# Kernel optimization log

Measured on AMD Instinct MI355X. Metric: run time of the kernel, lower is better.

## Reference

```python
import jax, jax.numpy as jnp
import numpy as np
from jax.scipy.special import logsumexp

SIGMA = 1.0
EPSILON = 1.0
MAX_ITER = 10


def _gaussian_kernel(x, y, sigma):
    # x: (b, l, d), y: (b, k, d) -> (b, l, k) negative-kernel matrix exp(-||x-y||^2 / (2 sigma^2))
    outer = jnp.einsum('bld,bkd->blk', x, y)
    norm_x = jnp.sum(x * x, axis=2)
    norm_y = jnp.sum(y * y, axis=2)
    dist = (norm_x[:, :, None] + norm_y[:, None, :] - 2.0 * outer) / (2.0 * sigma ** 2)
    return jnp.exp(-jnp.maximum(dist, 0.0))


def setup_inputs() -> dict:
    key = jax.random.key(0)
    kx, ka, ky, kb = jax.random.split(key, 4)
    B, L, K, D = 8, 2048, 2048, 32
    return {
        'x': jax.random.normal(kx, (B, L, D), dtype=jnp.float32),
        'a': jax.random.normal(ka, (B, L), dtype=jnp.float32),
        'y': jax.random.normal(ky, (B, K, D), dtype=jnp.float32),
        'b': jax.random.normal(kb, (B, K), dtype=jnp.float32),
    }


def _sinkhorn_potentials(x, a, y, b):
    sg = jax.lax.stop_gradient
    # Kernel matrices (carry gradient wrt x, y); weights a, b are detached inside kernels.
    Kxx = _gaussian_kernel(x, x, SIGMA) / EPSILON + sg(a)[:, None, :]
    Kyx_base = _gaussian_kernel(y, x, SIGMA)
    Kyx = Kyx_base / EPSILON + sg(a)[:, None, :]
    Kxy = jnp.swapaxes(Kyx_base, 1, 2) / EPSILON + sg(b)[:, None, :]
    Kyy = _gaussian_kernel(y, y, SIGMA) / EPSILON + sg(b)[:, None, :]

    # Sinkhorn loop runs under no_grad in the original: stop-gradient kernels.
    Kxx_s, Kyx_s, Kxy_s, Kyy_s = sg(Kxx), sg(Kyx), sg(Kxy), sg(Kyy)

    def step(carry, _):
        fxx, fyx, fxy, fyy = carry
        # sequential (Gauss-Seidel) update order matches the torch dict order xx, yx, xy, yy
        fxx = 0.5 * fxx - 0.5 * logsumexp(Kxx_s + fxx[:, None, :], axis=2)
        fyx = 0.5 * fyx - 0.5 * logsumexp(Kyx_s + fxy[:, None, :], axis=2)  # uses old fxy
        fxy = 0.5 * fxy - 0.5 * logsumexp(Kxy_s + fyx[:, None, :], axis=2)  # uses new fyx
        fyy = 0.5 * fyy - 0.5 * logsumexp(Kyy_s + fyy[:, None, :], axis=2)
        return (fxx, fyx, fxy, fyy), None

    init = (jnp.zeros_like(a), jnp.zeros_like(b), jnp.zeros_like(a), jnp.zeros_like(b))
    (fxx, fyx, fxy, fyy), _ = jax.lax.scan(step, init, None, length=MAX_ITER)

    # Final differentiable extrapolation step (potentials are detached constants).
    fe_xx = -logsumexp(Kxx + fxx[:, None, :], axis=2)
    fe_yx = -logsumexp(Kyx + fxy[:, None, :], axis=2)
    fe_xy = -logsumexp(Kxy + fyx[:, None, :], axis=2)
    fe_yy = -logsumexp(Kyy + fyy[:, None, :], axis=2)
    f = fe_xy - fe_xx  # (b, l)
    g = fe_yx - fe_yy  # (b, k)
    return f, g


def reference(x, a, y, b):
    f, g = _sinkhorn_potentials(x, a, y, b)
    res = jnp.sum(f * jnp.exp(a), axis=1) + jnp.sum(g * jnp.exp(b), axis=1)
    return res * EPSILON  # (batch,)
```

## Files before the change

kernel.cpp:

```cpp
#include <hip/hip_runtime.h>
#include <hip/hip_bf16.h>

#define B_ 8
#define N_ 2048
#define D_ 32
#define RCAP 16
#define EM1_DIAG 1.7182818284590452f
#define M_   8.0f
#define EM_  2980.9579870417283f
#define L2E  1.4426950408889634f
#define LN2  0.6931471805599453f
#define MH_  (0.5f * M_ * L2E)

typedef __attribute__((ext_vector_type(8))) short short8;
typedef __attribute__((ext_vector_type(4))) float f32x4;

__global__ void setup_kernel(const float* __restrict__ x, const float* __restrict__ y,
                             unsigned short* __restrict__ xb, unsigned short* __restrict__ yb,
                             float* __restrict__ NX, float* __restrict__ NY,
                             int* __restrict__ csr_cnt)
{
    int t = blockIdx.x * 256 + threadIdx.x;
    const float* src = (t < 16384) ? x : y;
    unsigned short* dstb = (t < 16384) ? xb : yb;
    float* dstn = (t < 16384) ? NX : NY;
    int row = (t < 16384) ? t : (t - 16384);
    const float4* p = reinterpret_cast<const float4*>(src + (size_t)row * D_);
    float ss = 0.f;
    float4 v[8];
    #pragma unroll
    for (int k = 0; k < 8; k++) {
        v[k] = p[k];
        ss += v[k].x * v[k].x + v[k].y * v[k].y + v[k].z * v[k].z + v[k].w * v[k].w;
    }
    short8* dst8 = reinterpret_cast<short8*>(dstb + (size_t)row * D_);
    #pragma unroll
    for (int k = 0; k < 4; k++) {
        const float fv[8] = { v[2*k].x, v[2*k].y, v[2*k].z, v[2*k].w,
                              v[2*k+1].x, v[2*k+1].y, v[2*k+1].z, v[2*k+1].w };
        short8 o;
        #pragma unroll
        for (int e = 0; e < 8; e++) {
            __hip_bfloat16 h = __float2bfloat16(fv[e]);
            o[e] = *reinterpret_cast<const short*>(&h);
        }
        dst8[k] = o;
    }
    dstn[row] = ss * 0.5f;
    csr_cnt[2 * t] = 0;
    csr_cnt[2 * t + 1] = 0;
}

__global__ __launch_bounds__(256) void discover_kernel(
    const unsigned short* __restrict__ xb, const unsigned short* __restrict__ yb,
    const float* __restrict__ NX, const float* __restrict__ NY,
    int* __restrict__ csr_cnt, uint2* __restrict__ csr_ent)
{
    int m = blockIdx.x >> 8;
    int rem = blockIdx.x & 255;
    int batch = rem >> 5;
    int rowblk = rem & 31;
    const unsigned short* rd = (m == 0) ? xb : yb;
    const float*          rN = (m == 0) ? NX : NY;
    const unsigned short* cd = (m == 1) ? yb : xb;
    const float*          cN = (m == 1) ? NY : NX;

    const int tid = threadIdx.x, lane = tid & 63, wv = tid >> 6;
    const int r0 = rowblk * 64;
    const size_t rowbase = (size_t)batch * N_ + r0;

    short8 afrag[4];
    f32x4 cinit[4];
    #pragma unroll
    for (int g = 0; g < 4; g++) {
        afrag[g] = *reinterpret_cast<const short8*>(
            rd + (rowbase + g * 16 + (lane & 15)) * D_ + (lane >> 4) * 8);
        float4 nv = *reinterpret_cast<const float4*>(
            rN + rowbase + g * 16 + (lane >> 4) * 4);
        cinit[g][0] = -nv.x; cinit[g][1] = -nv.y; cinit[g][2] = -nv.z; cinit[g][3] = -nv.w;
    }
    const unsigned short* cdB = cd + (size_t)batch * N_ * D_;
    const float* cNB = cN + batch * N_;
    const int c0w = wv * 512;

    unsigned mask = 0;
    #pragma unroll 8
    for (int cc = 0; cc < 32; ++cc) {
        int col = c0w + cc * 16 + (lane & 15);
        short8 bfrag = *reinterpret_cast<const short8*>(
            cdB + (size_t)col * D_ + (lane >> 4) * 8);
        float ny = cNB[col];
        f32x4 d[4];
        #pragma unroll
        for (int g = 0; g < 4; g++)
            d[g] = __builtin_amdgcn_mfma_f32_16x16x32_bf16(afrag[g], bfrag, cinit[g], 0, 0, 0);
        float m0 = fmaxf(fmaxf(d[0][0], d[0][1]), fmaxf(d[0][2], d[0][3]));
        float m1 = fmaxf(fmaxf(d[1][0], d[1][1]), fmaxf(d[1][2], d[1][3]));
        float m2 = fmaxf(fmaxf(d[2][0], d[2][1]), fmaxf(d[2][2], d[2][3]));
        float m3 = fmaxf(fmaxf(d[3][0], d[3][1]), fmaxf(d[3][2], d[3][3]));
        float mx = fmaxf(fmaxf(m0, m1), fmaxf(m2, m3));
        mask |= (__any(mx > ny - 10.0f) ? 1u : 0u) << cc;
    }

    auto push = [&](int T, int row, int colv, float em1) {
        size_t base = (size_t)(T * B_ + batch) * N_ + row;
        int idx = atomicAdd(&csr_cnt[base], 1);
        if (idx < RCAP)
            csr_ent[base * RCAP + idx] = make_uint2((unsigned)colv, __float_as_uint(em1));
    };
    while (mask) {
        int cc = __builtin_ctz(mask);
        mask &= mask - 1;
        int col = c0w + cc * 16 + (lane & 15);
        short8 bfrag = *reinterpret_cast<const short8*>(
            cdB + (size_t)col * D_ + (lane >> 4) * 8);
        float ny = cNB[col];
        f32x4 d[4];
        #pragma unroll
        for (int g = 0; g < 4; g++)
            d[g] = __builtin_amdgcn_mfma_f32_16x16x32_bf16(afrag[g], bfrag, cinit[g], 0, 0, 0);
        #pragma unroll
        for (int g = 0; g < 4; g++) {
            #pragma unroll
            for (int r = 0; r < 4; r++) {
                float dist = ny - d[g][r];
                if (dist < 10.0f) {
                    int i = r0 + g * 16 + (lane >> 4) * 4 + r;
                    if (m == 2) {
                        float em1 = __expf(__expf(-fmaxf(dist, 0.f))) - 1.0f;
                        push(2, i, col, em1);
                        push(3, col, i, em1);
                    } else if (i != col) {
                        float em1 = __expf(__expf(-fmaxf(dist, 0.f))) - 1.0f;
                        push(m, i, col, em1);
                    }
                }
            }
        }
    }
}

__global__ __launch_bounds__(1024) void sinkhorn_kernel(
    const float* __restrict__ a_in, const float* __restrict__ b_in,
    const int* __restrict__ csr_cnt, const uint2* __restrict__ csr_ent,
    float* __restrict__ out)
{
    __shared__ float evb[2][4][N_];
    __shared__ float Sacc[3][4];
    __shared__ float resacc;

    const int batch = blockIdx.x;
    const int t = threadIdx.x, lane = t & 63;

    int cnts[4][2];
    const uint2* ebase[4];
    #pragma unroll
    for (int T = 0; T < 4; T++) {
        size_t bb = (size_t)(T * B_ + batch) * N_;
        ebase[T] = csr_ent + bb * (size_t)RCAP;
        cnts[T][0] = min(csr_cnt[bb + t], RCAP);
        cnts[T][1] = min(csr_cnt[bb + t + 1024], RCAP);
    }
    float AW[2], BW[2];
    float F0[2] = {0.f, 0.f}, F1[2] = {0.f, 0.f}, F2[2] = {0.f, 0.f}, F3[2] = {0.f, 0.f};
    #pragma unroll
    for (int q = 0; q < 2; q++) {
        int j = t + 1024 * q;
        AW[q] = (a_in[batch * N_ + j] - M_) * L2E;
        BW[q] = (b_in[batch * N_ + j] - M_) * L2E;
    }
    if (t < 12) (&Sacc[0][0])[t] = 0.f;
    if (t == 0) resacc = 0.f;
    __syncthreads();

    auto gath = [&](const uint2* E, int cnt, const float* evbuf) -> float {
        float g = 0.f;
        for (int k = 0; k < cnt; ++k) {
            uint2 e = E[k];
            g += evbuf[e.x] * __uint_as_float(e.y);
        }
        return g;
    };
    auto wredadd = [&](float v, float* dst) {
        #pragma unroll
        for (int off = 1; off < 64; off <<= 1) v += __shfl_xor(v, off, 64);
        if (lane == 0) atomicAdd(dst, v);
    };

    auto stageA = [&](int s) {
        const int p2 = s & 1, p3 = s % 3, p3n = (s + 1) % 3;
        float e0q[2], e2q[2];
        float s0 = 0.f, s1 = 0.f, s2 = 0.f;
        #pragma unroll
        for (int q = 0; q < 2; q++) {
            int j = t + 1024 * q;
            float e0 = __builtin_amdgcn_exp2f(AW[q] + F0[q]); evb[p2][0][j] = e0; e0q[q] = e0; s0 += e0;
            float e1 = __builtin_amdgcn_exp2f(AW[q] + F2[q]); evb[p2][1][j] = e1;              s1 += e1;
            float e2 = __builtin_amdgcn_exp2f(BW[q] + F3[q]); evb[p2][2][j] = e2; e2q[q] = e2; s2 += e2;
        }
        wredadd(s0, &Sacc[p3][0]);
        wredadd(s1, &Sacc[p3][1]);
        wredadd(s2, &Sacc[p3][2]);
        if (t == 0) { Sacc[p3n][0] = 0.f; Sacc[p3n][1] = 0.f; Sacc[p3n][2] = 0.f; Sacc[p3n][3] = 0.f; }
        __syncthreads();
        float S0 = Sacc[p3][0], S1 = Sacc[p3][1], S2 = Sacc[p3][2];
        #pragma unroll
        for (int q = 0; q < 2; q++) {
            int i = t + 1024 * q;
            float g0 = gath(ebase[0] + (size_t)i * RCAP, cnts[0][q], evb[p2][0]);
            float g1 = gath(ebase[2] + (size_t)i * RCAP, cnts[2][q], evb[p2][1]);
            float g2 = gath(ebase[1] + (size_t)i * RCAP, cnts[1][q], evb[p2][2]);
            float lg0 = __builtin_amdgcn_logf(S0 + fmaf(e0q[q], EM1_DIAG, g0));
            float lg1 = __builtin_amdgcn_logf(S1 + g1);
            float lg2 = __builtin_amdgcn_logf(S2 + fmaf(e2q[q], EM1_DIAG, g2));
            F0[q] = fmaf(0.5f, F0[q], -fmaf(0.5f, lg0, MH_));
            F1[q] = fmaf(0.5f, F1[q], -fmaf(0.5f, lg1, MH_));
            F3[q] = fmaf(0.5f, F3[q], -fmaf(0.5f, lg2, MH_));
        }
    };

    auto stageB = [&](int s) {
        const int p2 = s & 1, p3 = s % 3, p3n = (s + 1) % 3;
        float sB = 0.f;
        #pragma unroll
        for (int q = 0; q < 2; q++) {
            int j = t + 1024 * q;
            float e = __builtin_amdgcn_exp2f(BW[q] + F1[q]); evb[p2][0][j] = e; sB += e;
        }
        wredadd(sB, &Sacc[p3][0]);
        if (t == 0) { Sacc[p3n][0] = 0.f; Sacc[p3n][1] = 0.f; Sacc[p3n][2] = 0.f; Sacc[p3n][3] = 0.f; }
        __syncthreads();
        float S = Sacc[p3][0];
        #pragma unroll
        for (int q = 0; q < 2; q++) {
            int i = t + 1024 * q;
            float g = gath(ebase[3] + (size_t)i * RCAP, cnts[3][q], evb[p2][0]);
            F2[q] = fmaf(0.5f, F2[q], -fmaf(0.5f, __builtin_amdgcn_logf(S + g), MH_));
        }
    };

    int s = 0;
    for (int it = 0; it < 10; ++it) {
        stageA(s); ++s;
        stageB(s); ++s;
    }

    {
        const int p2 = s & 1, p3 = s % 3;
        float e0q[2], e3q[2];
        float s0 = 0.f, s1 = 0.f, s2 = 0.f, s3 = 0.f;
        #pragma unroll
        for (int q = 0; q < 2; q++) {
            int j = t + 1024 * q;
            float e0 = __builtin_amdgcn_exp2f(AW[q] + F0[q]); evb[p2][0][j] = e0; e0q[q] = e0; s0 += e0;
            float e1 = __builtin_amdgcn_exp2f(AW[q] + F2[q]); evb[p2][1][j] = e1;              s1 += e1;
            float e2 = __builtin_amdgcn_exp2f(BW[q] + F1[q]); evb[p2][2][j] = e2;              s2 += e2;
            float e3 = __builtin_amdgcn_exp2f(BW[q] + F3[q]); evb[p2][3][j] = e3; e3q[q] = e3; s3 += e3;
        }
        wredadd(s0, &Sacc[p3][0]);
        wredadd(s1, &Sacc[p3][1]);
        wredadd(s2, &Sacc[p3][2]);
        wredadd(s3, &Sacc[p3][3]);
        __syncthreads();
        float S0 = Sacc[p3][0], S1 = Sacc[p3][1], S2 = Sacc[p3][2], S3 = Sacc[p3][3];
        float ctr = 0.f;
        #pragma unroll
        for (int q = 0; q < 2; q++) {
            int i = t + 1024 * q;
            float lg0 = __builtin_amdgcn_logf(S0 + fmaf(e0q[q], EM1_DIAG,
                            gath(ebase[0] + (size_t)i * RCAP, cnts[0][q], evb[p2][0])));
            float lg1 = __builtin_amdgcn_logf(S1 +
                            gath(ebase[2] + (size_t)i * RCAP, cnts[2][q], evb[p2][1]));
            float lg2 = __builtin_amdgcn_logf(S2 +
                            gath(ebase[3] + (size_t)i * RCAP, cnts[3][q], evb[p2][2]));
            float lg3 = __builtin_amdgcn_logf(S3 + fmaf(e3q[q], EM1_DIAG,
                            gath(ebase[1] + (size_t)i * RCAP, cnts[1][q], evb[p2][3])));
            float ea = __builtin_amdgcn_exp2f(AW[q]);
            float eb = __builtin_amdgcn_exp2f(BW[q]);
            ctr += (lg0 - lg2) * ea + (lg3 - lg1) * eb;
        }
        ctr *= (LN2 * EM_);
        #pragma unroll
        for (int off = 1; off < 64; off <<= 1) ctr += __shfl_xor(ctr, off, 64);
        if (lane == 0) atomicAdd(&resacc, ctr);
        __syncthreads();
        if (t == 0) out[batch] = resacc;
    }
}

extern "C" void kernel_launch(void* const* d_in, const int* in_sizes, int n_in,
                              void* d_out, int out_size, void* d_ws, size_t ws_size,
                              hipStream_t stream)
{
    const float* x = (const float*)d_in[0];
    const float* a = (const float*)d_in[1];
    const float* y = (const float*)d_in[2];
    const float* b = (const float*)d_in[3];
    float* out = (float*)d_out;

    char* ws = (char*)d_ws;
    size_t o = 0;
    unsigned short* xb = (unsigned short*)(ws + o); o += (size_t)B_ * N_ * D_ * 2;
    unsigned short* yb = (unsigned short*)(ws + o); o += (size_t)B_ * N_ * D_ * 2;
    float* NX = (float*)(ws + o); o += (size_t)B_ * N_ * 4;
    float* NY = (float*)(ws + o); o += (size_t)B_ * N_ * 4;
    int* csr_cnt = (int*)(ws + o); o += (size_t)4 * B_ * N_ * 4;
    uint2* csr_ent = (uint2*)(ws + o); o += (size_t)4 * B_ * N_ * RCAP * 8;

    setup_kernel<<<128, 256, 0, stream>>>(x, y, xb, yb, NX, NY, csr_cnt);
    discover_kernel<<<3 * 256, 256, 0, stream>>>(xb, yb, NX, NY, csr_cnt, csr_ent);
    sinkhorn_kernel<<<B_, 1024, 0, stream>>>(a, b, csr_cnt, csr_ent, out);
}
```

Measured before the change: 168.3 us.

## Split discover columns across more blocks, cache sparse entries, deterministic partial sums

The discover kernel now splits each row block's columns into four chunks, giving four times as many blocks with fewer columns per wave. This raises parallelism across the GPU. The sinkhorn kernel preloads the first two sparse entries per row into registers, so the iterations no longer reload them from global memory. It also replaces the shared-memory atomic sums with per-wave partial slots plus a fixed tree reduction, which removes the triple-buffer zeroing. The cost is more registers per thread and a deterministic but different summation order.

```diff
diff --git a/kernel.cpp b/kernel.cpp
--- a/kernel.cpp
+++ b/kernel.cpp
@@ -56,10 +56,12 @@
     const float* __restrict__ NX, const float* __restrict__ NY,
     int* __restrict__ csr_cnt, uint2* __restrict__ csr_ent)
 {
-    int m = blockIdx.x >> 8;
-    int rem = blockIdx.x & 255;
-    int batch = rem >> 5;
-    int rowblk = rem & 31;
+    int m = blockIdx.x >> 10;
+    int rem = blockIdx.x & 1023;
+    int batch = rem >> 7;
+    int rem2 = rem & 127;
+    int rowblk = rem2 >> 2;
+    int cchunk = rem2 & 3;
     const unsigned short* rd = (m == 0) ? xb : yb;
     const float*          rN = (m == 0) ? NX : NY;
     const unsigned short* cd = (m == 1) ? yb : xb;
@@ -81,11 +83,11 @@
     }
     const unsigned short* cdB = cd + (size_t)batch * N_ * D_;
     const float* cNB = cN + batch * N_;
-    const int c0w = wv * 512;
+    const int c0w = cchunk * 512 + wv * 128;
 
     unsigned mask = 0;
-    #pragma unroll 8
-    for (int cc = 0; cc < 32; ++cc) {
+    #pragma unroll
+    for (int cc = 0; cc < 8; ++cc) {
         int col = c0w + cc * 16 + (lane & 15);
         short8 bfrag = *reinterpret_cast<const short8*>(
             cdB + (size_t)col * D_ + (lane >> 4) * 8);
@@ -146,20 +148,28 @@
     float* __restrict__ out)
 {
     __shared__ float evb[2][4][N_];
-    __shared__ float Sacc[3][4];
+    __shared__ float Spart[2][4][16];
     __shared__ float resacc;
 
     const int batch = blockIdx.x;
-    const int t = threadIdx.x, lane = t & 63;
+    const int t = threadIdx.x, lane = t & 63, wv = t >> 6;
 
     int cnts[4][2];
     const uint2* ebase[4];
+    uint2 ec[4][2][2];
     #pragma unroll
     for (int T = 0; T < 4; T++) {
         size_t bb = (size_t)(T * B_ + batch) * N_;
         ebase[T] = csr_ent + bb * (size_t)RCAP;
-        cnts[T][0] = min(csr_cnt[bb + t], RCAP);
-        cnts[T][1] = min(csr_cnt[bb + t + 1024], RCAP);
+        #pragma unroll
+        for (int q = 0; q < 2; q++) {
+            int row = t + 1024 * q;
+            int c = min(csr_cnt[bb + row], RCAP);
+            cnts[T][q] = c;
+            const uint2* E = ebase[T] + (size_t)row * RCAP;
+            ec[T][q][0] = (c > 0) ? E[0] : make_uint2(0u, 0u);
+            ec[T][q][1] = (c > 1) ? E[1] : make_uint2(0u, 0u);
+        }
     }
     float AW[2], BW[2];
     float F0[2] = {0.f, 0.f}, F1[2] = {0.f, 0.f}, F2[2] = {0.f, 0.f}, F3[2] = {0.f, 0.f};
@@ -169,47 +179,54 @@
         AW[q] = (a_in[batch * N_ + j] - M_) * L2E;
         BW[q] = (b_in[batch * N_ + j] - M_) * L2E;
     }
-    if (t < 12) (&Sacc[0][0])[t] = 0.f;
     if (t == 0) resacc = 0.f;
     __syncthreads();
 
-    auto gath = [&](const uint2* E, int cnt, const float* evbuf) -> float {
+    auto gath = [&](int T, int q, const float* evbuf) -> float {
+        int c = cnts[T][q];
         float g = 0.f;
-        for (int k = 0; k < cnt; ++k) {
-            uint2 e = E[k];
-            g += evbuf[e.x] * __uint_as_float(e.y);
+        if (c > 0) g += evbuf[ec[T][q][0].x] * __uint_as_float(ec[T][q][0].y);
+        if (c > 1) g += evbuf[ec[T][q][1].x] * __uint_as_float(ec[T][q][1].y);
+        if (__builtin_expect(c > 2, 0)) {
+            const uint2* E = ebase[T] + (size_t)(t + 1024 * q) * RCAP;
+            for (int k = 2; k < c; ++k)
+                g += evbuf[E[k].x] * __uint_as_float(E[k].y);
         }
         return g;
     };
-    auto wredadd = [&](float v, float* dst) {
+    auto wpart = [&](float v, float* slot) {
         #pragma unroll
         for (int off = 1; off < 64; off <<= 1) v += __shfl_xor(v, off, 64);
-        if (lane == 0) atomicAdd(dst, v);
+        if (lane == 0) *slot = v;
+    };
+    auto tree16 = [](const float* r) -> float {
+        return (((r[0] + r[1]) + (r[2] + r[3])) + ((r[4] + r[5]) + (r[6] + r[7])))
+             + (((r[8] + r[9]) + (r[10] + r[11])) + ((r[12] + r[13]) + (r[14] + r[15])));
     };
 
     auto stageA = [&](int s) {
-        const int p2 = s & 1, p3 = s % 3, p3n = (s + 1) % 3;
+        const int p = s & 1;
         float e0q[2], e2q[2];
         float s0 = 0.f, s1 = 0.f, s2 = 0.f;
         #pragma unroll
         for (int q = 0; q < 2; q++) {
             int j = t + 1024 * q;
-            float e0 = __builtin_amdgcn_exp2f(AW[q] + F0[q]); evb[p2][0][j] = e0; e0q[q] = e0; s0 += e0;
-            float e1 = __builtin_amdgcn_exp2f(AW[q] + F2[q]); evb[p2][1][j] = e1;              s1 += e1;
-            float e2 = __builtin_amdgcn_exp2f(BW[q] + F3[q]); evb[p2][2][j] = e2; e2q[q] = e2; s2 += e2;
-        }
-        wredadd(s0, &Sacc[p3][0]);
-        wredadd(s1, &Sacc[p3][1]);
-        wredadd(s2, &Sacc[p3][2]);
-        if (t == 0) { Sacc[p3n][0] = 0.f; Sacc[p3n][1] = 0.f; Sacc[p3n][2] = 0.f; Sacc[p3n][3] = 0.f; }
+            float e0 = __builtin_amdgcn_exp2f(AW[q] + F0[q]); evb[p][0][j] = e0; e0q[q] = e0; s0 += e0;
+            float e1 = __builtin_amdgcn_exp2f(AW[q] + F2[q]); evb[p][1][j] = e1;              s1 += e1;
+            float e2 = __builtin_amdgcn_exp2f(BW[q] + F3[q]); evb[p][2][j] = e2; e2q[q] = e2; s2 += e2;
+        }
+        wpart(s0, &Spart[p][0][wv]);
+        wpart(s1, &Spart[p][1][wv]);
+        wpart(s2, &Spart[p][2][wv]);
         __syncthreads();
-        float S0 = Sacc[p3][0], S1 = Sacc[p3][1], S2 = Sacc[p3][2];
-        #pragma unroll
-        for (int q = 0; q < 2; q++) {
-            int i = t + 1024 * q;
-            float g0 = gath(ebase[0] + (size_t)i * RCAP, cnts[0][q], evb[p2][0]);
-            float g1 = gath(ebase[2] + (size_t)i * RCAP, cnts[2][q], evb[p2][1]);
-            float g2 = gath(ebase[1] + (size_t)i * RCAP, cnts[1][q], evb[p2][2]);
+        float S0 = tree16(Spart[p][0]);
+        float S1 = tree16(Spart[p][1]);
+        float S2 = tree16(Spart[p][2]);
+        #pragma unroll
+        for (int q = 0; q < 2; q++) {
+            float g0 = gath(0, q, evb[p][0]);
+            float g1 = gath(2, q, evb[p][1]);
+            float g2 = gath(1, q, evb[p][2]);
             float lg0 = __builtin_amdgcn_logf(S0 + fmaf(e0q[q], EM1_DIAG, g0));
             float lg1 = __builtin_amdgcn_logf(S1 + g1);
             float lg2 = __builtin_amdgcn_logf(S2 + fmaf(e2q[q], EM1_DIAG, g2));
@@ -220,21 +237,19 @@
     };
 
     auto stageB = [&](int s) {
-        const int p2 = s & 1, p3 = s % 3, p3n = (s + 1) % 3;
+        const int p = s & 1;
         float sB = 0.f;
         #pragma unroll
         for (int q = 0; q < 2; q++) {
             int j = t + 1024 * q;
-            float e = __builtin_amdgcn_exp2f(BW[q] + F1[q]); evb[p2][0][j] = e; sB += e;
-        }
-        wredadd(sB, &Sacc[p3][0]);
-        if (t == 0) { Sacc[p3n][0] = 0.f; Sacc[p3n][1] = 0.f; Sacc[p3n][2] = 0.f; Sacc[p3n][3] = 0.f; }
+            float e = __builtin_amdgcn_exp2f(BW[q] + F1[q]); evb[p][0][j] = e; sB += e;
+        }
+        wpart(sB, &Spart[p][0][wv]);
         __syncthreads();
-        float S = Sacc[p3][0];
-        #pragma unroll
-        for (int q = 0; q < 2; q++) {
-            int i = t + 1024 * q;
-            float g = gath(ebase[3] + (size_t)i * RCAP, cnts[3][q], evb[p2][0]);
+        float S = tree16(Spart[p][0]);
+        #pragma unroll
+        for (int q = 0; q < 2; q++) {
+            float g = gath(3, q, evb[p][0]);
             F2[q] = fmaf(0.5f, F2[q], -fmaf(0.5f, __builtin_amdgcn_logf(S + g), MH_));
         }
     };
@@ -246,35 +261,31 @@
     }
 
     {
-        const int p2 = s & 1, p3 = s % 3;
+        const int p = s & 1;
         float e0q[2], e3q[2];
         float s0 = 0.f, s1 = 0.f, s2 = 0.f, s3 = 0.f;
         #pragma unroll
         for (int q = 0; q < 2; q++) {
             int j = t + 1024 * q;
-            float e0 = __builtin_amdgcn_exp2f(AW[q] + F0[q]); evb[p2][0][j] = e0; e0q[q] = e0; s0 += e0;
-            float e1 = __builtin_amdgcn_exp2f(AW[q] + F2[q]); evb[p2][1][j] = e1;              s1 += e1;
-            float e2 = __builtin_amdgcn_exp2f(BW[q] + F1[q]); evb[p2][2][j] = e2;              s2 += e2;
-            float e3 = __builtin_amdgcn_exp2f(BW[q] + F3[q]); evb[p2][3][j] = e3; e3q[q] = e3; s3 += e3;
-        }
-        wredadd(s0, &Sacc[p3][0]);
-        wredadd(s1, &Sacc[p3][1]);
-        wredadd(s2, &Sacc[p3][2]);
-        wredadd(s3, &Sacc[p3][3]);
+            float e0 = __builtin_amdgcn_exp2f(AW[q] + F0[q]); evb[p][0][j] = e0; e0q[q] = e0; s0 += e0;
+            float e1 = __builtin_amdgcn_exp2f(AW[q] + F2[q]); evb[p][1][j] = e1;              s1 += e1;
+            float e2 = __builtin_amdgcn_exp2f(BW[q] + F1[q]); evb[p][2][j] = e2;              s2 += e2;
+            float e3 = __builtin_amdgcn_exp2f(BW[q] + F3[q]); evb[p][3][j] = e3; e3q[q] = e3; s3 += e3;
+        }
+        wpart(s0, &Spart[p][0][wv]);
+        wpart(s1, &Spart[p][1][wv]);
+        wpart(s2, &Spart[p][2][wv]);
+        wpart(s3, &Spart[p][3][wv]);
         __syncthreads();
-        float S0 = Sacc[p3][0], S1 = Sacc[p3][1], S2 = Sacc[p3][2], S3 = Sacc[p3][3];
+        float S0 = tree16(Spart[p][0]), S1 = tree16(Spart[p][1]);
+        float S2 = tree16(Spart[p][2]), S3 = tree16(Spart[p][3]);
         float ctr = 0.f;
         #pragma unroll
         for (int q = 0; q < 2; q++) {
-            int i = t + 1024 * q;
-            float lg0 = __builtin_amdgcn_logf(S0 + fmaf(e0q[q], EM1_DIAG,
-                            gath(ebase[0] + (size_t)i * RCAP, cnts[0][q], evb[p2][0])));
-            float lg1 = __builtin_amdgcn_logf(S1 +
-                            gath(ebase[2] + (size_t)i * RCAP, cnts[2][q], evb[p2][1]));
-            float lg2 = __builtin_amdgcn_logf(S2 +
-                            gath(ebase[3] + (size_t)i * RCAP, cnts[3][q], evb[p2][2]));
-            float lg3 = __builtin_amdgcn_logf(S3 + fmaf(e3q[q], EM1_DIAG,
-                            gath(ebase[1] + (size_t)i * RCAP, cnts[1][q], evb[p2][3])));
+            float lg0 = __builtin_amdgcn_logf(S0 + fmaf(e0q[q], EM1_DIAG, gath(0, q, evb[p][0])));
+            float lg1 = __builtin_amdgcn_logf(S1 + gath(2, q, evb[p][1]));
+            float lg2 = __builtin_amdgcn_logf(S2 + gath(3, q, evb[p][2]));
+            float lg3 = __builtin_amdgcn_logf(S3 + fmaf(e3q[q], EM1_DIAG, gath(1, q, evb[p][3])));
             float ea = __builtin_amdgcn_exp2f(AW[q]);
             float eb = __builtin_amdgcn_exp2f(BW[q]);
             ctr += (lg0 - lg2) * ea + (lg3 - lg1) * eb;
@@ -308,6 +319,6 @@
     uint2* csr_ent = (uint2*)(ws + o); o += (size_t)4 * B_ * N_ * RCAP * 8;
 
     setup_kernel<<<128, 256, 0, stream>>>(x, y, xb, yb, NX, NY, csr_cnt);
-    discover_kernel<<<3 * 256, 256, 0, stream>>>(xb, yb, NX, NY, csr_cnt, csr_ent);
+    discover_kernel<<<3 * 1024, 256, 0, stream>>>(xb, yb, NX, NY, csr_cnt, csr_ent);
     sinkhorn_kernel<<<B_, 1024, 0, stream>>>(a, b, csr_cnt, csr_ent, out);
 }
```

Result: slower. 176.2 us (+4.7%).
